# Kernel tuning notes

Measured on AMD Instinct MI355X. Metric: run time of the kernel, lower is better.

Reference implementation:

```python
import jax, jax.numpy as jnp
import numpy as np

N_AC = 8192     # number of amacrine cells
N_BC = 8192     # number of bipolar-cell helpers
T_KERNEL = 52   # len(torch.arange(0.8, 0, -1/64)) with input_frequency=64


def setup_inputs() -> dict:
    key = jax.random.key(0)
    k_x, k_w, k_k, k_s, k_o = jax.random.split(key, 5)
    x = jax.random.normal(k_x, (N_BC, T_KERNEL), dtype=jnp.float32)
    bc_ac_weight = jax.random.normal(k_w, (N_AC, N_BC), dtype=jnp.float32) / np.sqrt(N_BC)
    ac_kernel = jax.random.normal(k_k, (N_AC, T_KERNEL), dtype=jnp.float32)
    # normalize kernel rows like compute_ac_kernel does
    ac_kernel = ac_kernel / jnp.linalg.norm(ac_kernel, axis=1, keepdims=True)
    # slopes come from exp(log_slope) in the original -> keep positive
    ac_sigmoid_slope = jax.random.uniform(k_s, (N_AC,), dtype=jnp.float32) + 0.5
    ac_sigmoid_offset = 0.1 * jax.random.normal(k_o, (N_AC,), dtype=jnp.float32)
    return {
        "x": x,
        "bc_ac_weight": bc_ac_weight,
        "ac_kernel": ac_kernel,
        "ac_sigmoid_slope": ac_sigmoid_slope,
        "ac_sigmoid_offset": ac_sigmoid_offset,
    }


def reference(x, bc_ac_weight, ac_kernel, ac_sigmoid_slope, ac_sigmoid_offset):
    """One AC feedback step.

    x:                (nBC, T)   BC activity history window
    bc_ac_weight:     (nAC, nBC) precomputed (exp of log weights)
    ac_kernel:        (nAC, T)   precomputed normalized double-exp kernel
    ac_sigmoid_slope: (nAC,)
    ac_sigmoid_offset:(nAC,)
    returns:          (nAC,)
    """
    t_kernel = ac_kernel.shape[-1]
    y = bc_ac_weight @ x  # (nAC, T)
    if y.shape[-1] < t_kernel:  # static-shape left zero-pad as in F.pad
        y = jnp.pad(y, ((0, 0), (t_kernel - y.shape[-1], 0)))
    s = jnp.sum(ac_kernel * y, axis=1)  # temporal weighted sum -> (nAC,)
    # precomputed_sigmoid: sigmoid with per-cell slope and offset
    return jax.nn.sigmoid(ac_sigmoid_slope * (s - ac_sigmoid_offset))
```

## Files before the change

### kernel.cpp

```cpp
#include <hip/hip_runtime.h>
#include <hip/hip_bf16.h>
#include <math.h>

#define N_AC  8192
#define N_BC  8192
#define T_K   52
#define T_PAD 64

#define KSPLIT 16
#define KSEG   (N_BC / KSPLIT)
#define CHUNK  256
#define NCHUNK (KSEG / CHUNK)
#define RSTRIDE 264

typedef __bf16 bf16x8 __attribute__((ext_vector_type(8)));
typedef __bf16 bf16x4 __attribute__((ext_vector_type(4)));
typedef float  f32x4  __attribute__((ext_vector_type(4)));

__global__ void bpack_kernel(const float* __restrict__ x, __bf16* __restrict__ Bp) {
    int gid   = blockIdx.x * blockDim.x + threadIdx.x;
    int lane  = gid & 63;
    int group = gid >> 6;
    int kblock = group >> 2;
    int nt     = group & 3;
    int quad = lane >> 4;
    int l15  = lane & 15;
    int t  = nt * 16 + l15;
    int b0 = kblock * 32 + quad * 8;
    bf16x8 v;
    #pragma unroll
    for (int j = 0; j < 8; ++j) {
        float f = (t < T_K) ? x[(b0 + j) * T_K + t] : 0.0f;
        v[j] = (__bf16)f;
    }
    *(bf16x8*)(Bp + (size_t)group * 512 + lane * 8) = v;
}

__global__ __launch_bounds__(256, 4) void ac_gemm_kernel(
    const float*  __restrict__ W,
    const __bf16* __restrict__ Bp,
    const float*  __restrict__ kern,
    float*        __restrict__ partials)
{
    const int tid  = threadIdx.x;
    const int lane = tid & 63;
    const int wave = tid >> 6;
    const int quad = lane >> 4;
    const int l15  = lane & 15;
    const int a0   = blockIdx.x * 64 + wave * 16;
    const int ksub = blockIdx.y;
    const int kbeg = ksub * KSEG;

    __shared__ __bf16 As[4 * 16 * RSTRIDE];
    __bf16* tile = &As[wave * 16 * RSTRIDE];

    const float* wbase = W + (size_t)a0 * N_BC + lane * 4;

    f32x4 acc[4] = {};

    float4 pre[16];
    #pragma unroll
    for (int j = 0; j < 16; ++j)
        pre[j] = *(const float4*)(wbase + (size_t)j * N_BC + kbeg);

    for (int c = 0; c < NCHUNK; ++c) {
        const int kc = kbeg + c * CHUNK;

        #pragma unroll
        for (int j = 0; j < 16; ++j) {
            bf16x4 h;
            h[0] = (__bf16)pre[j].x; h[1] = (__bf16)pre[j].y;
            h[2] = (__bf16)pre[j].z; h[3] = (__bf16)pre[j].w;
            *(bf16x4*)&tile[j * RSTRIDE + lane * 4] = h;
        }

        if (c + 1 < NCHUNK) {
            #pragma unroll
            for (int j = 0; j < 16; ++j)
                pre[j] = *(const float4*)(wbase + (size_t)j * N_BC + kc + CHUNK);
        }

        #pragma unroll
        for (int s = 0; s < 8; ++s) {
            bf16x8 af = *(const bf16x8*)&tile[l15 * RSTRIDE + s * 32 + quad * 8];
            const size_t kblock = (size_t)(kc >> 5) + s;
            #pragma unroll
            for (int nt = 0; nt < 4; ++nt) {
                bf16x8 bf = *(const bf16x8*)(Bp + (kblock * 4 + nt) * 512 + lane * 8);
                acc[nt] = __builtin_amdgcn_mfma_f32_16x16x32_bf16(af, bf, acc[nt], 0, 0, 0);
            }
        }
    }

    float p[4] = {0.f, 0.f, 0.f, 0.f};
    #pragma unroll
    for (int nt = 0; nt < 4; ++nt) {
        int t = nt * 16 + l15;
        if (t < T_K) {
            #pragma unroll
            for (int r = 0; r < 4; ++r) {
                int grow = a0 + quad * 4 + r;
                p[r] += acc[nt][r] * kern[grow * T_K + t];
            }
        }
    }
    #pragma unroll
    for (int m = 1; m <= 8; m <<= 1) {
        #pragma unroll
        for (int r = 0; r < 4; ++r) p[r] += __shfl_xor(p[r], m);
    }

    if (l15 == 0) {
        #pragma unroll
        for (int r = 0; r < 4; ++r)
            partials[ksub * N_AC + a0 + quad * 4 + r] = p[r];
    }
}

__global__ void ac_final_kernel(const float* __restrict__ partials,
                                const float* __restrict__ slope,
                                const float* __restrict__ offs,
                                float* __restrict__ out) {
    int a = blockIdx.x * blockDim.x + threadIdx.x;
    if (a >= N_AC) return;
    float s = 0.f;
    #pragma unroll
    for (int ks = 0; ks < KSPLIT; ++ks) s += partials[ks * N_AC + a];
    float z = slope[a] * (s - offs[a]);
    out[a] = 1.0f / (1.0f + __expf(-z));
}

extern "C" void kernel_launch(void* const* d_in, const int* in_sizes, int n_in,
                              void* d_out, int out_size, void* d_ws, size_t ws_size,
                              hipStream_t stream) {
    const float* x     = (const float*)d_in[0];
    const float* W     = (const float*)d_in[1];
    const float* kern  = (const float*)d_in[2];
    const float* slope = (const float*)d_in[3];
    const float* offs  = (const float*)d_in[4];
    float* out = (float*)d_out;

    __bf16* Bp      = (__bf16*)d_ws;
    float* partials = (float*)((char*)d_ws + (size_t)1024 * 512 * sizeof(__bf16));

    bpack_kernel<<<dim3(65536 / 256), dim3(256), 0, stream>>>(x, Bp);
    ac_gemm_kernel<<<dim3(N_AC / 64, KSPLIT), dim3(256), 0, stream>>>(
        W, Bp, kern, partials);
    ac_final_kernel<<<dim3(N_AC / 256), dim3(256), 0, stream>>>(
        partials, slope, offs, out);
}
```

Baseline: 383.3 us.

## Load W directly in MFMA fragment layout and stage packed x in LDS

Doubles the K split to 32 so each block covers 256 columns. The packed bf16 x slice for that segment is staged once into shared memory, replacing repeated global loads of B fragments. Each lane now loads its W row segment straight in the MFMA A-operand layout (16 float4 registers) and converts it in registers, which removes the LDS transpose tile and the chunk loop. This cuts LDS traffic and the W staging step, but all W loads are issued up front with no software pipelining, there are more partials to reduce, and register pressure is higher.

```diff
diff --git a/kernel.cpp b/kernel.cpp
--- a/kernel.cpp
+++ b/kernel.cpp
@@ -7,14 +7,11 @@
 #define T_K   52
 #define T_PAD 64
 
-#define KSPLIT 16
+#define KSPLIT 32
 #define KSEG   (N_BC / KSPLIT)
-#define CHUNK  256
-#define NCHUNK (KSEG / CHUNK)
-#define RSTRIDE 264
+#define NKB    (KSEG / 32)
 
 typedef __bf16 bf16x8 __attribute__((ext_vector_type(8)));
-typedef __bf16 bf16x4 __attribute__((ext_vector_type(4)));
 typedef float  f32x4  __attribute__((ext_vector_type(4)));
 
 __global__ void bpack_kernel(const float* __restrict__ x, __bf16* __restrict__ Bp) {
@@ -51,44 +48,37 @@
     const int ksub = blockIdx.y;
     const int kbeg = ksub * KSEG;
 
-    __shared__ __bf16 As[4 * 16 * RSTRIDE];
-    __bf16* tile = &As[wave * 16 * RSTRIDE];
+    __shared__ __bf16 Bs[NKB * 4 * 512];
+    {
+        const __bf16* src = Bp + (size_t)(ksub * NKB * 4) * 512;
+        #pragma unroll
+        for (int j = 0; j < 8; ++j)
+            *(bf16x8*)(Bs + (j * 256 + tid) * 8) =
+                *(const bf16x8*)(src + (j * 256 + tid) * 8);
+    }
+    __syncthreads();
 
-    const float* wbase = W + (size_t)a0 * N_BC + lane * 4;
+    const float* wrow = W + (size_t)(a0 + l15) * N_BC + kbeg + quad * 8;
+    float4 pre[2 * NKB];
+    #pragma unroll
+    for (int s = 0; s < NKB; ++s) {
+        pre[2 * s]     = *(const float4*)(wrow + s * 32);
+        pre[2 * s + 1] = *(const float4*)(wrow + s * 32 + 4);
+    }
 
     f32x4 acc[4] = {};
 
-    float4 pre[16];
     #pragma unroll
-    for (int j = 0; j < 16; ++j)
-        pre[j] = *(const float4*)(wbase + (size_t)j * N_BC + kbeg);
-
-    for (int c = 0; c < NCHUNK; ++c) {
-        const int kc = kbeg + c * CHUNK;
-
+    for (int s = 0; s < NKB; ++s) {
+        bf16x8 af;
+        af[0] = (__bf16)pre[2*s].x;   af[1] = (__bf16)pre[2*s].y;
+        af[2] = (__bf16)pre[2*s].z;   af[3] = (__bf16)pre[2*s].w;
+        af[4] = (__bf16)pre[2*s+1].x; af[5] = (__bf16)pre[2*s+1].y;
+        af[6] = (__bf16)pre[2*s+1].z; af[7] = (__bf16)pre[2*s+1].w;
         #pragma unroll
-        for (int j = 0; j < 16; ++j) {
-            bf16x4 h;
-            h[0] = (__bf16)pre[j].x; h[1] = (__bf16)pre[j].y;
-            h[2] = (__bf16)pre[j].z; h[3] = (__bf16)pre[j].w;
-            *(bf16x4*)&tile[j * RSTRIDE + lane * 4] = h;
-        }
-
-        if (c + 1 < NCHUNK) {
-            #pragma unroll
-            for (int j = 0; j < 16; ++j)
-                pre[j] = *(const float4*)(wbase + (size_t)j * N_BC + kc + CHUNK);
-        }
-
-        #pragma unroll
-        for (int s = 0; s < 8; ++s) {
-            bf16x8 af = *(const bf16x8*)&tile[l15 * RSTRIDE + s * 32 + quad * 8];
-            const size_t kblock = (size_t)(kc >> 5) + s;
-            #pragma unroll
-            for (int nt = 0; nt < 4; ++nt) {
-                bf16x8 bf = *(const bf16x8*)(Bp + (kblock * 4 + nt) * 512 + lane * 8);
-                acc[nt] = __builtin_amdgcn_mfma_f32_16x16x32_bf16(af, bf, acc[nt], 0, 0, 0);
-            }
+        for (int nt = 0; nt < 4; ++nt) {
+            bf16x8 bf = *(const bf16x8*)(Bs + ((s * 4 + nt) * 512 + lane * 8));
+            acc[nt] = __builtin_amdgcn_mfma_f32_16x16x32_bf16(af, bf, acc[nt], 0, 0, 0);
         }
     }
 
```

Measured after the change: 387.3 us. Within noise of the previous version (+1.0%).
